# Kernel tuning notes

Hardware: AMD Instinct MI355X
Metric: run time of the kernel (lower is better)

Reference implementation:

```python
import jax, jax.numpy as jnp
import numpy as np

HEADS, DH = 8, 32

def _ln(x):
    m = x.mean(-1, keepdims=True)
    v = ((x - m) ** 2).mean(-1, keepdims=True)
    return (x - m) * jax.lax.rsqrt(v + 1e-5)

def _attn(xq, xk, ei, ea, wq, wk, wv, we, wo):
    # one relation: q from dst-type nodes xq, k/v from src-type nodes xk
    Nd, Ns, E = xq.shape[0], xk.shape[0], ea.shape[0]
    src, dst = ei[0], ei[1]
    q = (xq @ wq).reshape(Nd, HEADS, DH)
    k = (xk @ wk).reshape(Ns, HEADS, DH)
    v = (xk @ wv).reshape(Ns, HEADS, DH)
    e = (ea @ we).reshape(E, HEADS, DH)
    s = jnp.sum(q[dst] * (k[src] + e), axis=-1) * (DH ** -0.5)  # (E, heads)
    m = jax.ops.segment_max(s, dst, num_segments=Nd)
    m = jnp.where(jnp.isfinite(m), m, 0.0)
    ex = jnp.exp(s - m[dst])
    den = jax.ops.segment_sum(ex, dst, num_segments=Nd)
    msg = jax.ops.segment_sum(ex[:, :, None] * (v[src] + e), dst, num_segments=Nd)
    msg = msg / (den[:, :, None] + 1e-9)
    return msg.reshape(Nd, HEADS * DH) @ wo

def setup_inputs() -> dict:
    key = jax.random.key(0)
    ks = list(jax.random.split(key, 24))
    N, H, ED, L, F = 18432, 256, 64, 2, 512
    EA, ES = 294912, 65536
    nrm = lambda k, shp, s=1.0: jax.random.normal(k, shp, dtype=jnp.float32) * s
    inp = {}
    inp['all_feats_left'] = nrm(ks[0], (N, H))
    inp['all_feats_right'] = nrm(ks[1], (N, H))
    inp['ea_ll'] = nrm(ks[2], (EA, ED))
    inp['ea_rr'] = nrm(ks[3], (EA, ED))
    inp['ea_lr'] = nrm(ks[4], (ES, ED))
    inp['ea_rl'] = nrm(ks[5], (ES, ED))
    inp['ei_ll'] = jax.random.randint(ks[6], (2, EA), 0, N, dtype=jnp.int32)
    inp['ei_rr'] = jax.random.randint(ks[7], (2, EA), 0, N, dtype=jnp.int32)
    inp['ei_lr'] = jax.random.randint(ks[8], (2, ES), 0, N, dtype=jnp.int32)
    inp['ei_rl'] = jax.random.randint(ks[9], (2, ES), 0, N, dtype=jnp.int32)
    # relation order: 0=ll, 1=rr, 2=lr (src left -> dst right), 3=rl
    inp['Wq'] = nrm(ks[10], (L, 4, H, H), H ** -0.5)
    inp['Wk'] = nrm(ks[11], (L, 4, H, H), H ** -0.5)
    inp['Wv'] = nrm(ks[12], (L, 4, H, H), H ** -0.5)
    inp['We'] = nrm(ks[13], (L, 4, ED, H), ED ** -0.5)
    inp['Wo'] = nrm(ks[14], (L, 4, H, H), H ** -0.5)
    inp['ffn_w1'] = nrm(ks[15], (L, 2, H, F), H ** -0.5)
    inp['ffn_b1'] = jnp.zeros((L, 2, F), jnp.float32)
    inp['ffn_w2'] = nrm(ks[16], (L, 2, F, H), F ** -0.5)
    inp['ffn_b2'] = jnp.zeros((L, 2, H), jnp.float32)
    inp['head_w1'] = nrm(ks[17], (H, H), H ** -0.5)
    inp['head_b1'] = jnp.zeros((H,), jnp.float32)
    inp['head_w2'] = nrm(ks[18], (H, 7), H ** -0.5)
    inp['head_b2'] = jnp.zeros((7,), jnp.float32)
    inp['action_start'] = 2048  # slice(K, None), K current nodes per arm
    return inp

def reference(all_feats_left, all_feats_right, ea_ll, ea_rr, ea_lr, ea_rl,
              Wq, Wk, Wv, We, Wo, ffn_w1, ffn_b1, ffn_w2, ffn_b2,
              head_w1, head_b1, head_w2, head_b2,
              ei_ll, ei_rr, ei_lr, ei_rl, action_start):
    xl, xr = all_feats_left, all_feats_right
    L = Wq.shape[0]
    for l in range(L):
        agg_l = (_attn(xl, xl, ei_ll, ea_ll, Wq[l, 0], Wk[l, 0], Wv[l, 0], We[l, 0], Wo[l, 0])
                 + _attn(xl, xr, ei_rl, ea_rl, Wq[l, 3], Wk[l, 3], Wv[l, 3], We[l, 3], Wo[l, 3]))
        agg_r = (_attn(xr, xr, ei_rr, ea_rr, Wq[l, 1], Wk[l, 1], Wv[l, 1], We[l, 1], Wo[l, 1])
                 + _attn(xr, xl, ei_lr, ea_lr, Wq[l, 2], Wk[l, 2], Wv[l, 2], We[l, 2], Wo[l, 2]))
        xl = _ln(xl + agg_l)
        xr = _ln(xr + agg_r)
        xl = _ln(xl + jax.nn.gelu(xl @ ffn_w1[l, 0] + ffn_b1[l, 0]) @ ffn_w2[l, 0] + ffn_b2[l, 0])
        xr = _ln(xr + jax.nn.gelu(xr @ ffn_w1[l, 1] + ffn_b1[l, 1]) @ ffn_w2[l, 1] + ffn_b2[l, 1])
    la = xl[action_start:]
    ra = xr[action_start:]
    head = lambda z: jax.nn.gelu(z @ head_w1 + head_b1) @ head_w2 + head_b2
    return head(la), head(ra)
```

## Files before the change

### kernel.cpp

```cpp
#include <hip/hip_runtime.h>
#include <math.h>

typedef __attribute__((ext_vector_type(8))) short short8;
typedef __attribute__((ext_vector_type(4))) float f32x4;

__device__ __forceinline__ unsigned short f2bf(float f) {
  unsigned u = __builtin_bit_cast(unsigned, f);
  u += 0x7fff + ((u >> 16) & 1);
  return (unsigned short)(u >> 16);
}
__device__ __forceinline__ float bf2f(unsigned short h) {
  unsigned u = ((unsigned)h) << 16;
  return __builtin_bit_cast(float, u);
}
__device__ __forceinline__ float gelu_f(float x) {
  const float c0 = 0.7978845608028654f;
  return 0.5f * x * (1.0f + tanhf(c0 * (x + 0.044715f * x * x * x)));
}
__device__ __forceinline__ void gload16(const unsigned short* g, unsigned short* l) {
  __builtin_amdgcn_global_load_lds(
      (const __attribute__((address_space(1))) unsigned int*)g,
      (__attribute__((address_space(3))) unsigned int*)l, 16, 0, 0);
}
__device__ __forceinline__ int ileave512(int cc) {
  const int base = (cc & 256) ? 4 : 0;
  const int c2 = cc & 255;
  return (c2 >> 2) * 8 + base + (c2 & 3);
}

__global__ __launch_bounds__(256)
void gemm_qkv_k(const unsigned short* __restrict__ A0, const unsigned short* __restrict__ A1,
                const unsigned short* __restrict__ BT0, const unsigned short* __restrict__ BT1,
                unsigned short* __restrict__ qT0, unsigned short* __restrict__ qT1,
                unsigned short* __restrict__ kvS0, unsigned short* __restrict__ kvS1,
                unsigned short* __restrict__ kvX0, unsigned short* __restrict__ kvX1,
                int M)
{
  const int z = blockIdx.z;
  const unsigned short* A  = z ? A1  : A0;
  const unsigned short* BT = z ? BT1 : BT0;
  unsigned short* qT  = z ? qT1  : qT0;
  unsigned short* kvS = z ? kvS1 : kvS0;
  unsigned short* kvX = z ? kvX1 : kvX0;
  const int K = 256, lda = 256;

  __shared__ __align__(16) unsigned short As[128 * 32];
  __shared__ __align__(16) unsigned short Bs[128 * 32];
  const int tid = threadIdx.x;
  const int bm = blockIdx.x * 128, bn = blockIdx.y * 128;
  const int lane = tid & 63, w = tid >> 6;
  const int wr = w >> 1, wc = w & 1;
  const int l15 = lane & 15, kg = lane >> 4;
  const int srow0 = w * 16 + (lane >> 2);
  const int srow1 = 64 + srow0;
  const int sslot = lane & 3;
  const int koff0 = (((sslot - (srow0 >> 1)) & 3)) * 8;
  const int koff1 = (((sslot - (srow1 >> 1)) & 3)) * 8;
  const unsigned short* gA0 = A + (size_t)(bm + srow0) * lda + koff0;
  const unsigned short* gA1 = A + (size_t)(bm + srow1) * lda + koff1;
  const unsigned short* gB0 = BT + (size_t)(bn + srow0) * K + koff0;
  const unsigned short* gB1 = BT + (size_t)(bn + srow1) * K + koff1;
  unsigned short* lA0 = As + w * 512;
  unsigned short* lA1 = As + 2048 + w * 512;
  unsigned short* lB0 = Bs + w * 512;
  unsigned short* lB1 = Bs + 2048 + w * 512;

  int roffA[4], roffB[4];
#pragma unroll
  for (int m = 0; m < 4; ++m) {
    int row = wr * 64 + m * 16 + l15;
    roffA[m] = row * 32 + ((kg + (row >> 1)) & 3) * 8;
  }
#pragma unroll
  for (int n = 0; n < 4; ++n) {
    int col = wc * 64 + n * 16 + l15;
    roffB[n] = col * 32 + ((kg + (col >> 1)) & 3) * 8;
  }

  f32x4 acc[4][4] = {};
  for (int k0 = 0; k0 < K; k0 += 32) {
    gload16(gA0 + k0, lA0);
    gload16(gA1 + k0, lA1);
    gload16(gB0 + k0, lB0);
    gload16(gB1 + k0, lB1);
    __syncthreads();
    short8 af[4], bfr[4];
#pragma unroll
    for (int m = 0; m < 4; ++m) af[m] = *(const short8*)(As + roffA[m]);
#pragma unroll
    for (int n = 0; n < 4; ++n) bfr[n] = *(const short8*)(Bs + roffB[n]);
#pragma unroll
    for (int m = 0; m < 4; ++m)
#pragma unroll
      for (int n = 0; n < 4; ++n)
        acc[m][n] = __builtin_amdgcn_mfma_f32_16x16x32_bf16(af[m], bfr[n], acc[m][n], 0, 0, 0);
    __syncthreads();
  }
#pragma unroll
  for (int m = 0; m < 4; ++m) {
#pragma unroll
    for (int n = 0; n < 4; ++n) {
      int col = bn + wc * 64 + n * 16 + l15;
      f32x4 v = acc[m][n];
#pragma unroll
      for (int r2 = 0; r2 < 4; ++r2) {
        int row = bm + wr * 64 + m * 16 + kg * 4 + r2;
        unsigned short bv = f2bf(v[r2]);
        if (col < 768) {
          qT[(size_t)row * 1536 + col] = bv;
        } else if (col < 1280) {
          kvS[(size_t)row * 512 + ileave512(col - 768)] = bv;
        } else if (col < 2048) {
          qT[(size_t)row * 1536 + 768 + (col - 1280)] = bv;
        } else {
          kvX[(size_t)row * 512 + ileave512(col - 2048)] = bv;
        }
      }
    }
  }
}

template<bool BIAS, bool GELU>
__global__ __launch_bounds__(256)
void gemm_mfma2_k(const unsigned short* __restrict__ A0, const unsigned short* __restrict__ A1,
                  int lda,
                  const unsigned short* __restrict__ BT0, const unsigned short* __restrict__ BT1,
                  const float* __restrict__ bias0, const float* __restrict__ bias1,
                  float* __restrict__ Cf0, float* __restrict__ Cf1, int Sf, int ldf,
                  unsigned short* __restrict__ Cb10, unsigned short* __restrict__ Cb11,
                  int S2, int ldb1,
                  unsigned short* __restrict__ Cb20, unsigned short* __restrict__ Cb21, int ldb2,
                  int M, int N, int K)
{
  const int z = blockIdx.z;
  const unsigned short* A  = z ? A1  : A0;
  const unsigned short* BT = z ? BT1 : BT0;
  const float* bias        = z ? bias1 : bias0;
  float* Cf                = z ? Cf1 : Cf0;
  unsigned short* Cb1      = z ? Cb11 : Cb10;
  unsigned short* Cb2      = z ? Cb21 : Cb20;

  __shared__ __align__(16) unsigned short As[128 * 32];
  __shared__ __align__(16) unsigned short Bs[128 * 32];
  const int tid = threadIdx.x;
  const int bm = blockIdx.x * 128, bn = blockIdx.y * 128;
  const int lane = tid & 63, w = tid >> 6;
  const int wr = w >> 1, wc = w & 1;
  const int l15 = lane & 15, kg = lane >> 4;
  const int srow0 = w * 16 + (lane >> 2);
  const int srow1 = 64 + srow0;
  const int sslot = lane & 3;
  const int koff0 = (((sslot - (srow0 >> 1)) & 3)) * 8;
  const int koff1 = (((sslot - (srow1 >> 1)) & 3)) * 8;
  const unsigned short* gA0 = A + (size_t)(bm + srow0) * lda + koff0;
  const unsigned short* gA1 = A + (size_t)(bm + srow1) * lda + koff1;
  const unsigned short* gB0 = BT + (size_t)(bn + srow0) * K + koff0;
  const unsigned short* gB1 = BT + (size_t)(bn + srow1) * K + koff1;
  unsigned short* lA0 = As + w * 512;
  unsigned short* lA1 = As + 2048 + w * 512;
  unsigned short* lB0 = Bs + w * 512;
  unsigned short* lB1 = Bs + 2048 + w * 512;

  int roffA[4], roffB[4];
#pragma unroll
  for (int m = 0; m < 4; ++m) {
    int row = wr * 64 + m * 16 + l15;
    roffA[m] = row * 32 + ((kg + (row >> 1)) & 3) * 8;
  }
#pragma unroll
  for (int n = 0; n < 4; ++n) {
    int col = wc * 64 + n * 16 + l15;
    roffB[n] = col * 32 + ((kg + (col >> 1)) & 3) * 8;
  }

  f32x4 acc[4][4] = {};
  for (int k0 = 0; k0 < K; k0 += 32) {
    gload16(gA0 + k0, lA0);
    gload16(gA1 + k0, lA1);
    gload16(gB0 + k0, lB0);
    gload16(gB1 + k0, lB1);
    __syncthreads();
    short8 af[4], bfr[4];
#pragma unroll
    for (int m = 0; m < 4; ++m) af[m] = *(const short8*)(As + roffA[m]);
#pragma unroll
    for (int n = 0; n < 4; ++n) bfr[n] = *(const short8*)(Bs + roffB[n]);
#pragma unroll
    for (int m = 0; m < 4; ++m)
#pragma unroll
      for (int n = 0; n < 4; ++n)
        acc[m][n] = __builtin_amdgcn_mfma_f32_16x16x32_bf16(af[m], bfr[n], acc[m][n], 0, 0, 0);
    __syncthreads();
  }
#pragma unroll
  for (int m = 0; m < 4; ++m) {
#pragma unroll
    for (int n = 0; n < 4; ++n) {
      int col = bn + wc * 64 + n * 16 + l15;
      float bv = BIAS ? bias[col] : 0.f;
      f32x4 v = acc[m][n];
#pragma unroll
      for (int r2 = 0; r2 < 4; ++r2) {
        int row = bm + wr * 64 + m * 16 + kg * 4 + r2;
        float val = v[r2] + bv;
        if (GELU) val = gelu_f(val);
        if (col < Sf) {
          Cf[(size_t)row * ldf + col] = val;
        } else if (col < S2) {
          Cb1[(size_t)row * ldb1 + (col - Sf)] = f2bf(val);
        } else {
          Cb2[(size_t)row * ldb2 + (col - S2)] = f2bf(val);
        }
      }
    }
  }
}

template<bool BIAS>
__global__ __launch_bounds__(256)
void gemm_k2(const float* __restrict__ A0, const float* __restrict__ A1,
             const float* __restrict__ B, const float* __restrict__ bias,
             float* __restrict__ C0, float* __restrict__ C1,
             int M, int N, int K)
{
  const float* A = blockIdx.z ? A1 : A0;
  float* C = blockIdx.z ? C1 : C0;
  __shared__ float As[16][132];
  __shared__ float Bs[16][132];
  const int tid = threadIdx.x;
  const int tx = tid & 15, ty = tid >> 4;
  const int bm = blockIdx.x * 128;
  float acc[8][8];
#pragma unroll
  for (int i = 0; i < 8; ++i)
#pragma unroll
    for (int j = 0; j < 8; ++j) acc[i][j] = 0.f;
  const int ar = tid >> 1;
  const int ac = (tid & 1) * 8;
  const int br = tid >> 4;
  const int bc = (tid & 15) * 8;
  for (int k0 = 0; k0 < K; k0 += 16) {
    {
      float av[8] = {0,0,0,0,0,0,0,0};
      if (bm + ar < M) {
        const float* app = A + (size_t)(bm + ar) * K + (k0 + ac);
        float4 a0 = *(const float4*)app;
        float4 a1 = *(const float4*)(app + 4);
        av[0]=a0.x; av[1]=a0.y; av[2]=a0.z; av[3]=a0.w;
        av[4]=a1.x; av[5]=a1.y; av[6]=a1.z; av[7]=a1.w;
      }
#pragma unroll
      for (int i = 0; i < 8; ++i) As[ac + i][ar] = av[i];
    }
    {
      float bv[8] = {0,0,0,0,0,0,0,0};
      const float* bpp = B + (size_t)(k0 + br) * N + bc;
#pragma unroll
      for (int i = 0; i < 8; ++i) { if (bc + i < N) bv[i] = bpp[i]; }
#pragma unroll
      for (int i = 0; i < 8; ++i) Bs[br][bc + i] = bv[i];
    }
    __syncthreads();
#pragma unroll
    for (int kk = 0; kk < 16; ++kk) {
      float a[8], b[8];
      float4 t0 = *(const float4*)&As[kk][ty * 8];
      float4 t1 = *(const float4*)&As[kk][ty * 8 + 4];
      float4 u0 = *(const float4*)&Bs[kk][tx * 8];
      float4 u1 = *(const float4*)&Bs[kk][tx * 8 + 4];
      a[0]=t0.x;a[1]=t0.y;a[2]=t0.z;a[3]=t0.w;a[4]=t1.x;a[5]=t1.y;a[6]=t1.z;a[7]=t1.w;
      b[0]=u0.x;b[1]=u0.y;b[2]=u0.z;b[3]=u0.w;b[4]=u1.x;b[5]=u1.y;b[6]=u1.z;b[7]=u1.w;
#pragma unroll
      for (int i = 0; i < 8; ++i)
#pragma unroll
        for (int j = 0; j < 8; ++j)
          acc[i][j] = fmaf(a[i], b[j], acc[i][j]);
    }
    __syncthreads();
  }
#pragma unroll
  for (int i = 0; i < 8; ++i) {
    int row = bm + ty * 8 + i;
    if (row >= M) continue;
    int colg = tx * 8;
    float* cp = C + (size_t)row * N + colg;
#pragma unroll
    for (int j = 0; j < 8; ++j) {
      int cc = colg + j;
      if (cc < N) {
        float val = acc[i][j];
        if (BIAS) val += bias[cc];
        cp[j] = val;
      }
    }
  }
}

__global__ void tc_k(const float* __restrict__ in, unsigned short* __restrict__ out,
                     int K, int N, int inStride, int outStride, int rowOff, int totK, int kOff)
{
  const int mat = blockIdx.y;
  const int idx = blockIdx.x * 256 + threadIdx.x;
  if (idx >= N * K) return;
  const int n = idx / K, k = idx - n * K;
  out[(size_t)mat * outStride + (size_t)(rowOff + n) * totK + kOff + k] =
      f2bf(in[(size_t)mat * inStride + (size_t)k * N + n]);
}

__global__ void tc_all_k(const float* __restrict__ Wq, const float* __restrict__ Wk,
                         const float* __restrict__ Wv, unsigned short* __restrict__ BTall)
{
  const int part = blockIdx.z;
  const int slot = blockIdx.y;
  const int l = slot >> 1, zz = slot & 1;
  const int self = l * 4 + zz;
  const int crossq = l * 4 + (zz ? 2 : 3);
  const int crosskv = l * 4 + (zz ? 3 : 2);
  const float* in; int mat, rowOff;
  switch (part) {
    case 0: in = Wq; mat = self;    rowOff = 0;    break;
    case 1: in = Wk; mat = self;    rowOff = 768;  break;
    case 2: in = Wv; mat = self;    rowOff = 1024; break;
    case 3: in = Wq; mat = crossq;  rowOff = 1280; break;
    case 4: in = Wk; mat = crosskv; rowOff = 2048; break;
    default:in = Wv; mat = crosskv; rowOff = 2304; break;
  }
  const int idx = blockIdx.x * 256 + threadIdx.x;
  const int n = idx >> 8, k = idx & 255;
  BTall[(size_t)slot * 655360 + (size_t)(rowOff + n) * 256 + k] =
      f2bf(in[(size_t)mat * 65536 + (size_t)k * 256 + n]);
}

__global__ __launch_bounds__(256)
void wqe2_k(unsigned short* __restrict__ BTall, const float* __restrict__ We)
{
  const int which = blockIdx.z;
  const int slot = blockIdx.y;
  const int l = slot >> 1, zz = slot & 1;
  const int mat = which ? (l * 4 + (zz ? 2 : 3)) : (l * 4 + zz);
  const int baseQ = which ? 1280 : 0;
  const int baseT = which ? 1536 : 256;
  const int oc = blockIdx.x;
  const int g = oc >> 6, cc = oc & 63;
  const int kin = threadIdx.x;
  const float* wrow = We + (size_t)mat * 16384 + (size_t)cc * 256 + g * 32;
  const unsigned short* bq = BTall + (size_t)slot * 655360 + (size_t)(baseQ + g * 32) * 256 + kin;
  float acc = 0.f;
#pragma unroll 8
  for (int d = 0; d < 32; ++d)
    acc += bf2f(bq[(size_t)d * 256]) * wrow[d];
  BTall[(size_t)slot * 655360 + (size_t)(baseT + oc) * 256 + kin] = f2bf(acc);
}

__global__ void wo_tc_k(const float* __restrict__ Wo, unsigned short* __restrict__ BTwoF)
{
  const int mat = blockIdx.y;
  const int idx = blockIdx.x * 256 + threadIdx.x;
  const int n = idx >> 8, k = idx & 255;
  const int l = mat >> 2, i = mat & 3;
  const int side = (i == 1 || i == 2) ? 1 : 0;
  const int base = (i >= 2) ? 768 : 0;
  BTwoF[(size_t)(l * 2 + side) * 393216 + (size_t)n * 1536 + base + k] =
      f2bf(Wo[(size_t)mat * 65536 + (size_t)k * 256 + n]);
}

__global__ __launch_bounds__(256)
void wc_k(const float* __restrict__ We, const float* __restrict__ Wo,
          unsigned short* __restrict__ BTwoF)
{
  const int mat = blockIdx.y;
  const int j = blockIdx.x;
  const int h = j >> 6, c = j & 63;
  const int n = threadIdx.x;
  const float* wep = We + (size_t)mat * 16384 + (size_t)c * 256 + h * 32;
  const float* wop = Wo + (size_t)mat * 65536 + (size_t)(h * 32) * 256 + n;
  float acc = 0.f;
#pragma unroll 8
  for (int d = 0; d < 32; ++d)
    acc += wep[d] * wop[(size_t)d * 256];
  const int l = mat >> 2, i = mat & 3;
  const int side = (i == 1 || i == 2) ? 1 : 0;
  const int base = (i >= 2) ? 768 : 0;
  BTwoF[(size_t)(l * 2 + side) * 393216 + (size_t)n * 1536 + base + 256 + j] = f2bf(acc);
}

__global__ __launch_bounds__(256)
void edge4_k(const int* __restrict__ o0, const int* __restrict__ o1,
             const int* __restrict__ o2, const int* __restrict__ o3,
             const int2* __restrict__ p0, const int2* __restrict__ p1,
             const int2* __restrict__ p2, const int2* __restrict__ p3,
             const float* __restrict__ e0, const float* __restrict__ e1,
             const float* __restrict__ e2, const float* __restrict__ e3,
             unsigned short* q0, unsigned short* q1,
             unsigned short* q2, unsigned short* q3,
             const unsigned short* __restrict__ k0, const unsigned short* __restrict__ k1,
             const unsigned short* __restrict__ k2, const unsigned short* __restrict__ k3,
             int Nn)
{
  const int y = blockIdx.y;
  const int* offs = (y == 0) ? o0 : (y == 1) ? o1 : (y == 2) ? o2 : o3;
  const int2* pairs = (y == 0) ? p0 : (y == 1) ? p1 : (y == 2) ? p2 : p3;
  const float* ea = (y == 0) ? e0 : (y == 1) ? e1 : (y == 2) ? e2 : e3;
  unsigned short* qTmsg = (y == 0) ? q0 : (y == 1) ? q1 : (y == 2) ? q2 : q3;
  const unsigned short* kv = (y == 0) ? k0 : (y == 1) ? k1 : (y == 2) ? k2 : k3;
  const int wv = (blockIdx.x * blockDim.x + threadIdx.x) >> 6;
  if (wv >= Nn) return;
  const int lane = threadIdx.x & 63;
  const int g = lane >> 3, p = lane & 7;
  const float scale = 0.17677669529663687f;
  const ushort4 qu = *(const ushort4*)(qTmsg + (size_t)wv * 1536 + lane * 4);
  const float qx = bf2f(qu.x), qy = bf2f(qu.y), qz = bf2f(qu.z), qw = bf2f(qu.w);
  const unsigned short* Tp = qTmsg + (size_t)wv * 1536 + 256 + g * 64 + p * 8;
  const ushort4 tu0 = *(const ushort4*)Tp;
  const ushort4 tu1 = *(const ushort4*)(Tp + 4);
  const float Ta0 = bf2f(tu0.x), Ta1 = bf2f(tu0.y), Ta2 = bf2f(tu0.z), Ta3 = bf2f(tu0.w);
  const float Tc0 = bf2f(tu1.x), Tc1 = bf2f(tu1.y), Tc2 = bf2f(tu1.z), Tc3 = bf2f(tu1.w);
  float m = -INFINITY, den = 0.f;
  float ax = 0.f, ay = 0.f, az = 0.f, aw = 0.f;
  float G[8] = {0,0,0,0,0,0,0,0};
  const int e0i = __builtin_amdgcn_readfirstlane(offs[wv]);
  const int e1i = __builtin_amdgcn_readfirstlane(offs[wv + 1]);
  for (int j = e0i; j < e1i; j += 2) {
    const bool hasB = (j + 1) < e1i;
    const int2 prA = pairs[j];
    const int2 prB = hasB ? pairs[j + 1] : prA;
    const f32x4* epA = (const f32x4*)(ea + (size_t)prA.x * 64 + p * 8);
    const f32x4* epB = (const f32x4*)(ea + (size_t)prB.x * 64 + p * 8);
    const f32x4 a0 = __builtin_nontemporal_load(epA);
    const f32x4 a1 = __builtin_nontemporal_load(epA + 1);
    const f32x4 b0 = __builtin_nontemporal_load(epB);
    const f32x4 b1 = __builtin_nontemporal_load(epB + 1);
    const short8 kvA = *(const short8*)(kv + (size_t)prA.y * 512 + lane * 8);
    const short8 kvB = *(const short8*)(kv + (size_t)prB.y * 512 + lane * 8);
    float pA = qx * bf2f((unsigned short)kvA[0]) + qy * bf2f((unsigned short)kvA[1])
             + qz * bf2f((unsigned short)kvA[2]) + qw * bf2f((unsigned short)kvA[3]);
    pA += a0[0]*Ta0 + a0[1]*Ta1 + a0[2]*Ta2 + a0[3]*Ta3;
    pA += a1[0]*Tc0 + a1[1]*Tc1 + a1[2]*Tc2 + a1[3]*Tc3;
    float pB = qx * bf2f((unsigned short)kvB[0]) + qy * bf2f((unsigned short)kvB[1])
             + qz * bf2f((unsigned short)kvB[2]) + qw * bf2f((unsigned short)kvB[3]);
    pB += b0[0]*Ta0 + b0[1]*Ta1 + b0[2]*Ta2 + b0[3]*Ta3;
    pB += b1[0]*Tc0 + b1[1]*Tc1 + b1[2]*Tc2 + b1[3]*Tc3;
    pA += __shfl_xor(pA, 1, 64); pA += __shfl_xor(pA, 2, 64); pA += __shfl_xor(pA, 4, 64);
    pB += __shfl_xor(pB, 1, 64); pB += __shfl_xor(pB, 2, 64); pB += __shfl_xor(pB, 4, 64);
    const float sA = pA * scale;
    const float sB = hasB ? pB * scale : -INFINITY;
    const float mn = fmaxf(m, fmaxf(sA, sB));
    const float corr = __expf(m - mn);
    const float wA = __expf(sA - mn);
    const float wB = __expf(sB - mn);
    m = mn;
    den = den * corr + wA + wB;
    ax = ax * corr + wA * bf2f((unsigned short)kvA[4]) + wB * bf2f((unsigned short)kvB[4]);
    ay = ay * corr + wA * bf2f((unsigned short)kvA[5]) + wB * bf2f((unsigned short)kvB[5]);
    az = az * corr + wA * bf2f((unsigned short)kvA[6]) + wB * bf2f((unsigned short)kvB[6]);
    aw = aw * corr + wA * bf2f((unsigned short)kvA[7]) + wB * bf2f((unsigned short)kvB[7]);
    G[0] = G[0] * corr + wA * a0[0] + wB * b0[0];
    G[1] = G[1] * corr + wA * a0[1] + wB * b0[1];
    G[2] = G[2] * corr + wA * a0[2] + wB * b0[2];
    G[3] = G[3] * corr + wA * a0[3] + wB * b0[3];
    G[4] = G[4] * corr + wA * a1[0] + wB * b1[0];
    G[5] = G[5] * corr + wA * a1[1] + wB * b1[1];
    G[6] = G[6] * corr + wA * a1[2] + wB * b1[2];
    G[7] = G[7] * corr + wA * a1[3] + wB * b1[3];
  }
  const float inv = 1.f / (den + 1e-9f);
  ushort4 o;
  o.x = f2bf(ax * inv); o.y = f2bf(ay * inv);
  o.z = f2bf(az * inv); o.w = f2bf(aw * inv);
  *(ushort4*)(qTmsg + (size_t)wv * 1536 + lane * 4) = o;
  short8 gn;
#pragma unroll
  for (int i = 0; i < 8; ++i) gn[i] = (short)f2bf(G[i] * inv);
  *(short8*)(qTmsg + (size_t)wv * 1536 + 256 + g * 64 + p * 8) = gn;
}

__global__ __launch_bounds__(256)
void add_ln2_k(unsigned short* __restrict__ xbL, const unsigned short* __restrict__ addL,
               unsigned short* __restrict__ xbR, const unsigned short* __restrict__ addR, int Nn)
{
  unsigned short* xb = blockIdx.y ? xbR : xbL;
  const unsigned short* add = blockIdx.y ? addR : addL;
  const int wv = (blockIdx.x * blockDim.x + threadIdx.x) >> 6;
  if (wv >= Nn) return;
  const int lane = threadIdx.x & 63;
  ushort4 xu = *(const ushort4*)(xb + (size_t)wv * 256 + lane * 4);
  ushort4 au = *(const ushort4*)(add + (size_t)wv * 256 + lane * 4);
  float4 y;
  y.x = bf2f(xu.x) + bf2f(au.x); y.y = bf2f(xu.y) + bf2f(au.y);
  y.z = bf2f(xu.z) + bf2f(au.z); y.w = bf2f(xu.w) + bf2f(au.w);
  float s = y.x + y.y + y.z + y.w;
#pragma unroll
  for (int msk = 1; msk < 64; msk <<= 1) s += __shfl_xor(s, msk, 64);
  const float mean = s * (1.f / 256.f);
  float4 d;
  d.x = y.x - mean; d.y = y.y - mean; d.z = y.z - mean; d.w = y.w - mean;
  float sq = d.x*d.x + d.y*d.y + d.z*d.z + d.w*d.w;
#pragma unroll
  for (int msk = 1; msk < 64; msk <<= 1) sq += __shfl_xor(sq, msk, 64);
  const float r = rsqrtf(sq * (1.f / 256.f) + 1e-5f);
  ushort4 ob;
  ob.x = f2bf(d.x * r); ob.y = f2bf(d.y * r);
  ob.z = f2bf(d.z * r); ob.w = f2bf(d.w * r);
  *(ushort4*)(xb + (size_t)wv * 256 + lane * 4) = ob;
}

__global__ void cvt_x2_k(const float* __restrict__ aL, unsigned short* __restrict__ xbL,
                         const float* __restrict__ aR, unsigned short* __restrict__ xbR, int n4)
{
  const float* a = blockIdx.y ? aR : aL;
  unsigned short* xb = blockIdx.y ? xbR : xbL;
  int i = blockIdx.x * 256 + threadIdx.x;
  if (i >= n4) return;
  float4 v = ((const float4*)a)[i];
  ushort4 b;
  b.x = f2bf(v.x); b.y = f2bf(v.y); b.z = f2bf(v.z); b.w = f2bf(v.w);
  ((ushort4*)xb)[i] = b;
}

__global__ void zero4_k(int* p, int n) {
  int i = blockIdx.x * 256 + threadIdx.x;
  if (i < n) p[i] = 0;
}
__global__ void hist4_k(const int* d0, const int* d1, const int* d2, const int* d3,
                        int E0, int E1, int E2, int E3, int* cnt, int Nn) {
  const int s = blockIdx.y;
  const int* d = (s == 0) ? d0 : (s == 1) ? d1 : (s == 2) ? d2 : d3;
  const int E = (s == 0) ? E0 : (s == 1) ? E1 : (s == 2) ? E2 : E3;
  int e = blockIdx.x * 256 + threadIdx.x;
  if (e < E) atomicAdd(&cnt[s * Nn + d[e]], 1);
}
__global__ __launch_bounds__(256)
void scan4_k(const int* __restrict__ cnt, int* __restrict__ offs, int* __restrict__ cursor, int Nn)
{
  __shared__ int sums[256];
  const int s = blockIdx.x;
  const int t = threadIdx.x;
  const int* c = cnt + (size_t)s * Nn;
  int* o = offs + (size_t)s * (Nn + 1);
  int* cur = cursor + (size_t)s * Nn;
  const int chunk = (Nn + 255) / 256;
  const int base = t * chunk;
  int sl = 0;
  for (int i = 0; i < chunk; ++i) {
    int idx = base + i;
    if (idx < Nn) sl += c[idx];
  }
  sums[t] = sl;
  __syncthreads();
  for (int off = 1; off < 256; off <<= 1) {
    int val = (t >= off) ? sums[t - off] : 0;
    __syncthreads();
    sums[t] += val;
    __syncthreads();
  }
  int run = (t == 0) ? 0 : sums[t - 1];
  for (int i = 0; i < chunk; ++i) {
    int idx = base + i;
    if (idx < Nn) { o[idx] = run; cur[idx] = run; run += c[idx]; }
  }
  if (t == 255) o[Nn] = run;
}
__global__ void scatter4_k(const int* e0p, const int* e1p, const int* e2p, const int* e3p,
                           int E0, int E1, int E2, int E3, int* cursor,
                           int2* p0, int2* p1, int2* p2, int2* p3, int Nn) {
  const int s = blockIdx.y;
  const int* ei = (s == 0) ? e0p : (s == 1) ? e1p : (s == 2) ? e2p : e3p;
  int2* po = (s == 0) ? p0 : (s == 1) ? p1 : (s == 2) ? p2 : p3;
  const int E = (s == 0) ? E0 : (s == 1) ? E1 : (s == 2) ? E2 : E3;
  int e = blockIdx.x * 256 + threadIdx.x;
  if (e < E) {
    int pos = atomicAdd(&cursor[s * Nn + ei[E + e]], 1);
    po[pos] = make_int2(e, ei[e]);
  }
}

extern "C" void kernel_launch(void* const* d_in, const int* in_sizes, int n_in,
                              void* d_out, int out_size, void* d_ws, size_t ws_size,
                              hipStream_t stream)
{
  (void)n_in; (void)ws_size;
  const float* afl = (const float*)d_in[0];
  const float* afr = (const float*)d_in[1];
  const float* eaA[4] = {(const float*)d_in[2], (const float*)d_in[3],
                         (const float*)d_in[4], (const float*)d_in[5]};
  const int* eiA[4] = {(const int*)d_in[6], (const int*)d_in[7],
                       (const int*)d_in[8], (const int*)d_in[9]};
  const float* Wq  = (const float*)d_in[10];
  const float* Wk  = (const float*)d_in[11];
  const float* Wv  = (const float*)d_in[12];
  const float* We  = (const float*)d_in[13];
  const float* Wo  = (const float*)d_in[14];
  const float* fw1 = (const float*)d_in[15];
  const float* fb1 = (const float*)d_in[16];
  const float* fw2 = (const float*)d_in[17];
  const float* fb2 = (const float*)d_in[18];
  const float* hw1 = (const float*)d_in[19];
  const float* hb1 = (const float*)d_in[20];
  const float* hw2 = (const float*)d_in[21];
  const float* hb2 = (const float*)d_in[22];

  const int Nn = in_sizes[0] / 256;
  const int E[4] = {in_sizes[2] / 64, in_sizes[3] / 64, in_sizes[4] / 64, in_sizes[5] / 64};
  const int Mh = out_size / 14;
  const int astart = Nn - Mh;
  float* out = (float*)d_out;

  char* wsp = (char*)d_ws;
  auto alloc = [&](size_t bytes) -> void* {
    void* pp = (void*)wsp;
    wsp += (bytes + 255) & ~(size_t)255;
    return pp;
  };
  unsigned short* xlb = (unsigned short*)alloc((size_t)Nn * 256 * 2);
  unsigned short* xrb = (unsigned short*)alloc((size_t)Nn * 256 * 2);
  unsigned short* aggLb = (unsigned short*)alloc((size_t)Nn * 256 * 2);
  unsigned short* aggRb = (unsigned short*)alloc((size_t)Nn * 256 * 2);
  unsigned short* qTmsgA = (unsigned short*)alloc((size_t)Nn * 1536 * 2);
  unsigned short* qTmsgB = (unsigned short*)alloc((size_t)Nn * 1536 * 2);
  unsigned short* kvSA = (unsigned short*)alloc((size_t)Nn * 512 * 2);
  unsigned short* kvSB = (unsigned short*)alloc((size_t)Nn * 512 * 2);
  unsigned short* kvXL = (unsigned short*)alloc((size_t)Nn * 512 * 2);
  unsigned short* kvXR = (unsigned short*)alloc((size_t)Nn * 512 * 2);
  unsigned short* BTall = (unsigned short*)alloc((size_t)4 * 655360 * 2);
  unsigned short* BTwoF = (unsigned short*)alloc((size_t)4 * 256 * 1536 * 2);
  unsigned short* BTf1  = (unsigned short*)alloc((size_t)4 * 512 * 256 * 2);
  unsigned short* BTf2  = (unsigned short*)alloc((size_t)4 * 256 * 512 * 2);
  unsigned short* BTh1  = (unsigned short*)alloc((size_t)256 * 256 * 2);
  int* offs4 = (int*)alloc((size_t)4 * (Nn + 1) * 4);
  int* cnt4  = (int*)alloc((size_t)4 * Nn * 4);
  int* cur4  = (int*)alloc((size_t)4 * Nn * 4);
  int2* pairs[4];
  for (int s = 0; s < 4; ++s) pairs[s] = (int2*)alloc((size_t)E[s] * 8);

  const dim3 B256(256);
  const int wgNodes = (Nn * 64 + 255) / 256;
  int maxE = E[0];
  for (int s = 1; s < 4; ++s) if (E[s] > maxE) maxE = E[s];

  cvt_x2_k<<<dim3((Nn * 64 + 255) / 256, 2), B256, 0, stream>>>(afl, xlb, afr, xrb, Nn * 64);
  zero4_k<<<dim3((4 * Nn + 255) / 256), B256, 0, stream>>>(cnt4, 4 * Nn);
  {
    dim3 gh((maxE + 255) / 256, 4);
    hist4_k<<<gh, B256, 0, stream>>>(eiA[0] + E[0], eiA[1] + E[1], eiA[2] + E[2], eiA[3] + E[3],
                                     E[0], E[1], E[2], E[3], cnt4, Nn);
    scan4_k<<<dim3(4), B256, 0, stream>>>(cnt4, offs4, cur4, Nn);
    scatter4_k<<<gh, B256, 0, stream>>>(eiA[0], eiA[1], eiA[2], eiA[3],
                                        E[0], E[1], E[2], E[3], cur4,
                                        pairs[0], pairs[1], pairs[2], pairs[3], Nn);
  }
  {
    tc_all_k<<<dim3(256, 4, 6), B256, 0, stream>>>(Wq, Wk, Wv, BTall);
    wqe2_k<<<dim3(512, 4, 2), B256, 0, stream>>>(BTall, We);
    wo_tc_k<<<dim3(256, 8), B256, 0, stream>>>(Wo, BTwoF);
    wc_k<<<dim3(512, 8), B256, 0, stream>>>(We, Wo, BTwoF);
    tc_k<<<dim3((131072 + 255) / 256, 4), B256, 0, stream>>>(fw1, BTf1, 256, 512, 131072, 131072, 0, 256, 0);
    tc_k<<<dim3((131072 + 255) / 256, 4), B256, 0, stream>>>(fw2, BTf2, 512, 256, 131072, 131072, 0, 512, 0);
    tc_k<<<dim3((65536 + 255) / 256, 1), B256, 0, stream>>>(hw1, BTh1, 256, 256, 0, 0, 0, 256, 0);
  }

  auto mfma2 = [&](const unsigned short* A0, const unsigned short* A1, int lda,
                   const unsigned short* BT0, const unsigned short* BT1,
                   const float* bias0, const float* bias1,
                   float* Cf0, float* Cf1, int Sf, int ldf,
                   unsigned short* Cb10, unsigned short* Cb11, int S2, int ldb1,
                   unsigned short* Cb20, unsigned short* Cb21, int ldb2,
                   int M, int N, int K, bool biasf, bool gelu) {
    dim3 g(M / 128, N / 128, 2);
    if (biasf && gelu)
      gemm_mfma2_k<true, true ><<<g, B256, 0, stream>>>(A0, A1, lda, BT0, BT1, bias0, bias1,
          Cf0, Cf1, Sf, ldf, Cb10, Cb11, S2, ldb1, Cb20, Cb21, ldb2, M, N, K);
    else if (biasf)
      gemm_mfma2_k<true, false><<<g, B256, 0, stream>>>(A0, A1, lda, BT0, BT1, bias0, bias1,
          Cf0, Cf1, Sf, ldf, Cb10, Cb11, S2, ldb1, Cb20, Cb21, ldb2, M, N, K);
    else
      gemm_mfma2_k<false, false><<<g, B256, 0, stream>>>(A0, A1, lda, BT0, BT1, bias0, bias1,
          Cf0, Cf1, Sf, ldf, Cb10, Cb11, S2, ldb1, Cb20, Cb21, ldb2, M, N, K);
  };

  for (int l = 0; l < 2; ++l) {
    gemm_qkv_k<<<dim3(Nn / 128, 20, 2), B256, 0, stream>>>(
        xlb, xrb,
        BTall + (size_t)(l * 2 + 0) * 655360, BTall + (size_t)(l * 2 + 1) * 655360,
        qTmsgA, qTmsgB, kvSA, kvSB, kvXL, kvXR, Nn);
    edge4_k<<<dim3(wgNodes, 4), B256, 0, stream>>>(
        offs4, offs4 + (size_t)(Nn + 1), offs4 + (size_t)3 * (Nn + 1), offs4 + (size_t)2 * (Nn + 1),
        pairs[0], pairs[1], pairs[3], pairs[2],
        eaA[0], eaA[1], eaA[3], eaA[2],
        qTmsgA, qTmsgB, qTmsgA + 768, qTmsgB + 768,
        kvSA, kvSB, kvXR, kvXL, Nn);
    mfma2(qTmsgA, qTmsgB, 1536, BTwoF + (size_t)(l*2+0)*393216, BTwoF + (size_t)(l*2+1)*393216,
          nullptr, nullptr, nullptr, nullptr, 0, 0, aggLb, aggRb, 256, 256,
          nullptr, nullptr, 0, Nn, 256, 1536, false, false);
    add_ln2_k<<<dim3(wgNodes, 2), B256, 0, stream>>>(xlb, aggLb, xrb, aggRb, Nn);
    const int fL = l * 2 + 0, fR = l * 2 + 1;
    mfma2(xlb, xrb, 256, BTf1 + (size_t)fL*131072, BTf1 + (size_t)fR*131072,
          fb1 + (size_t)fL*512, fb1 + (size_t)fR*512, nullptr, nullptr, 0, 0,
          kvSA, kvSB, 512, 512, nullptr, nullptr, 0, Nn, 512, 256, true, true);
    mfma2(kvSA, kvSB, 512, BTf2 + (size_t)fL*131072, BTf2 + (size_t)fR*131072,
          fb2 + (size_t)fL*256, fb2 + (size_t)fR*256, nullptr, nullptr, 0, 0,
          aggLb, aggRb, 256, 256, nullptr, nullptr, 0, Nn, 256, 512, true, false);
    add_ln2_k<<<dim3(wgNodes, 2), B256, 0, stream>>>(xlb, aggLb, xrb, aggRb, Nn);
  }
  float* h1L = (float*)kvSA;
  float* h1R = (float*)kvSB;
  mfma2(xlb + (size_t)astart * 256, xrb + (size_t)astart * 256, 256, BTh1, BTh1,
        hb1, hb1, h1L, h1R, 256, 256, nullptr, nullptr, 0, 0, nullptr, nullptr, 0,
        Mh, 256, 256, true, true);
  gemm_k2<true><<<dim3(Mh / 128, 1, 2), B256, 0, stream>>>(h1L, h1R, hw2, hb2,
                                                           out, out + (size_t)Mh * 7, Mh, 7, 256);
}
```

Measured before the change: 1.057 ms.

## Double-buffer LDS tiles in GEMM k-loops to overlap loads with MFMA

Both bf16 MFMA GEMM kernels now use a shared k-loop helper that double-buffers the A/B LDS tiles. The next k-slice is issued via global_load_lds before the current slice is consumed, with an explicit vmcnt wait and raw barriers. This is meant to hide global-load latency behind the matrix math instead of stalling at every step. In exchange, LDS use doubles to 32 KB per block, which may lower occupancy, and correctness depends on the hand-written vmcnt counts.

```diff
diff --git a/kernel.cpp b/kernel.cpp
--- a/kernel.cpp
+++ b/kernel.cpp
@@ -26,6 +26,60 @@
   const int base = (cc & 256) ? 4 : 0;
   const int c2 = cc & 255;
   return (c2 >> 2) * 8 + base + (c2 & 3);
+}
+
+__device__ __forceinline__ void kloop_db(
+    const unsigned short* gA0, const unsigned short* gA1,
+    const unsigned short* gB0, const unsigned short* gB1,
+    unsigned short* As, unsigned short* Bs,
+    int lo0, int lo1, const int* roffA, const int* roffB,
+    f32x4 (&acc)[4][4], int K)
+{
+  gload16(gA0, As + lo0);
+  gload16(gA1, As + lo1);
+  gload16(gB0, Bs + lo0);
+  gload16(gB1, Bs + lo1);
+  int cur = 0;
+  for (int k0 = 32; k0 < K; k0 += 32) {
+    const int nb = (cur ^ 1) * 4096;
+    gload16(gA0 + k0, As + nb + lo0);
+    gload16(gA1 + k0, As + nb + lo1);
+    gload16(gB0 + k0, Bs + nb + lo0);
+    gload16(gB1 + k0, Bs + nb + lo1);
+    __builtin_amdgcn_sched_barrier(0);
+    asm volatile("s_waitcnt vmcnt(4)" ::: "memory");
+    __builtin_amdgcn_s_barrier();
+    __builtin_amdgcn_sched_barrier(0);
+    const int cb = cur * 4096;
+    short8 af[4], bfr[4];
+#pragma unroll
+    for (int m = 0; m < 4; ++m) af[m] = *(const short8*)(As + cb + roffA[m]);
+#pragma unroll
+    for (int n = 0; n < 4; ++n) bfr[n] = *(const short8*)(Bs + cb + roffB[n]);
+#pragma unroll
+    for (int m = 0; m < 4; ++m)
+#pragma unroll
+      for (int n = 0; n < 4; ++n)
+        acc[m][n] = __builtin_amdgcn_mfma_f32_16x16x32_bf16(af[m], bfr[n], acc[m][n], 0, 0, 0);
+    __builtin_amdgcn_sched_barrier(0);
+    __builtin_amdgcn_s_barrier();
+    cur ^= 1;
+  }
+  __builtin_amdgcn_sched_barrier(0);
+  asm volatile("s_waitcnt vmcnt(0)" ::: "memory");
+  __builtin_amdgcn_s_barrier();
+  __builtin_amdgcn_sched_barrier(0);
+  const int cb = cur * 4096;
+  short8 af[4], bfr[4];
+#pragma unroll
+  for (int m = 0; m < 4; ++m) af[m] = *(const short8*)(As + cb + roffA[m]);
+#pragma unroll
+  for (int n = 0; n < 4; ++n) bfr[n] = *(const short8*)(Bs + cb + roffB[n]);
+#pragma unroll
+  for (int m = 0; m < 4; ++m)
+#pragma unroll
+    for (int n = 0; n < 4; ++n)
+      acc[m][n] = __builtin_amdgcn_mfma_f32_16x16x32_bf16(af[m], bfr[n], acc[m][n], 0, 0, 0);
 }
 
 __global__ __launch_bounds__(256)
@@ -44,8 +98,8 @@
   unsigned short* kvX = z ? kvX1 : kvX0;
   const int K = 256, lda = 256;
 
-  __shared__ __align__(16) unsigned short As[128 * 32];
-  __shared__ __align__(16) unsigned short Bs[128 * 32];
+  __shared__ __align__(16) unsigned short As[2 * 4096];
+  __shared__ __align__(16) unsigned short Bs[2 * 4096];
   const int tid = threadIdx.x;
   const int bm = blockIdx.x * 128, bn = blockIdx.y * 128;
   const int lane = tid & 63, w = tid >> 6;
@@ -60,10 +114,8 @@
   const unsigned short* gA1 = A + (size_t)(bm + srow1) * lda + koff1;
   const unsigned short* gB0 = BT + (size_t)(bn + srow0) * K + koff0;
   const unsigned short* gB1 = BT + (size_t)(bn + srow1) * K + koff1;
-  unsigned short* lA0 = As + w * 512;
-  unsigned short* lA1 = As + 2048 + w * 512;
-  unsigned short* lB0 = Bs + w * 512;
-  unsigned short* lB1 = Bs + 2048 + w * 512;
+  const int lo0 = w * 512;
+  const int lo1 = 2048 + w * 512;
 
   int roffA[4], roffB[4];
 #pragma unroll
@@ -78,24 +130,8 @@
   }
 
   f32x4 acc[4][4] = {};
-  for (int k0 = 0; k0 < K; k0 += 32) {
-    gload16(gA0 + k0, lA0);
-    gload16(gA1 + k0, lA1);
-    gload16(gB0 + k0, lB0);
-    gload16(gB1 + k0, lB1);
-    __syncthreads();
-    short8 af[4], bfr[4];
-#pragma unroll
-    for (int m = 0; m < 4; ++m) af[m] = *(const short8*)(As + roffA[m]);
-#pragma unroll
-    for (int n = 0; n < 4; ++n) bfr[n] = *(const short8*)(Bs + roffB[n]);
-#pragma unroll
-    for (int m = 0; m < 4; ++m)
-#pragma unroll
-      for (int n = 0; n < 4; ++n)
-        acc[m][n] = __builtin_amdgcn_mfma_f32_16x16x32_bf16(af[m], bfr[n], acc[m][n], 0, 0, 0);
-    __syncthreads();
-  }
+  kloop_db(gA0, gA1, gB0, gB1, As, Bs, lo0, lo1, roffA, roffB, acc, K);
+
 #pragma unroll
   for (int m = 0; m < 4; ++m) {
 #pragma unroll
@@ -140,8 +176,8 @@
   unsigned short* Cb1      = z ? Cb11 : Cb10;
   unsigned short* Cb2      = z ? Cb21 : Cb20;
 
-  __shared__ __align__(16) unsigned short As[128 * 32];
-  __shared__ __align__(16) unsigned short Bs[128 * 32];
+  __shared__ __align__(16) unsigned short As[2 * 4096];
+  __shared__ __align__(16) unsigned short Bs[2 * 4096];
   const int tid = threadIdx.x;
   const int bm = blockIdx.x * 128, bn = blockIdx.y * 128;
   const int lane = tid & 63, w = tid >> 6;
@@ -156,10 +192,8 @@
   const unsigned short* gA1 = A + (size_t)(bm + srow1) * lda + koff1;
   const unsigned short* gB0 = BT + (size_t)(bn + srow0) * K + koff0;
   const unsigned short* gB1 = BT + (size_t)(bn + srow1) * K + koff1;
-  unsigned short* lA0 = As + w * 512;
-  unsigned short* lA1 = As + 2048 + w * 512;
-  unsigned short* lB0 = Bs + w * 512;
-  unsigned short* lB1 = Bs + 2048 + w * 512;
+  const int lo0 = w * 512;
+  const int lo1 = 2048 + w * 512;
 
   int roffA[4], roffB[4];
 #pragma unroll
@@ -174,24 +208,8 @@
   }
 
   f32x4 acc[4][4] = {};
-  for (int k0 = 0; k0 < K; k0 += 32) {
-    gload16(gA0 + k0, lA0);
-    gload16(gA1 + k0, lA1);
-    gload16(gB0 + k0, lB0);
-    gload16(gB1 + k0, lB1);
-    __syncthreads();
-    short8 af[4], bfr[4];
-#pragma unroll
-    for (int m = 0; m < 4; ++m) af[m] = *(const short8*)(As + roffA[m]);
-#pragma unroll
-    for (int n = 0; n < 4; ++n) bfr[n] = *(const short8*)(Bs + roffB[n]);
-#pragma unroll
-    for (int m = 0; m < 4; ++m)
-#pragma unroll
-      for (int n = 0; n < 4; ++n)
-        acc[m][n] = __builtin_amdgcn_mfma_f32_16x16x32_bf16(af[m], bfr[n], acc[m][n], 0, 0, 0);
-    __syncthreads();
-  }
+  kloop_db(gA0, gA1, gB0, gB1, As, Bs, lo0, lo1, roffA, roffB, acc, K);
+
 #pragma unroll
   for (int m = 0; m < 4; ++m) {
 #pragma unroll
```

Result: faster. 1.029 ms (-2.7%).
